# Optimization experiments

Measured on AMD Instinct MI355X. Metric: run time of the kernel, lower is better.

Reference implementation:

```python
import jax, jax.numpy as jnp
import numpy as np

N_NODES = 50000
N_EDGES = 800000
EMB = 128
HID = [128, 128]
OUT = 64
CE = 8  # stand-in for CROSS_ENTROPY_INDEXES: first 8 output columns get sigmoid


def _linear_params(key, d_in, d_out):
    k1, k2 = jax.random.split(key)
    s = 1.0 / np.sqrt(d_in)
    w = jax.random.uniform(k1, (d_in, d_out), minval=-s, maxval=s, dtype=jnp.float32)
    b = jax.random.uniform(k2, (d_out,), minval=-s, maxval=s, dtype=jnp.float32)
    return w, b


def setup_inputs() -> dict:
    key = jax.random.key(0)
    ks = jax.random.split(key, 16)
    z = jax.random.normal(ks[0], (N_NODES, EMB), dtype=jnp.float32)
    edge_index = jax.random.randint(ks[1], (2, N_EDGES), 0, N_NODES, dtype=jnp.int64)
    # SAGEConv params: neighbor weight (with bias) + root weight
    w1_n, b1 = _linear_params(ks[2], EMB, HID[0])
    w1_r, _ = _linear_params(ks[3], EMB, HID[0])
    w2_n, b2 = _linear_params(ks[4], HID[0], HID[1])
    w2_r, _ = _linear_params(ks[5], HID[0], HID[1])
    wf_n, bf = _linear_params(ks[6], HID[1], OUT)
    wf_r, _ = _linear_params(ks[7], HID[1], OUT)
    # initial residual linears: emb -> hid[1], emb -> out
    w_res1, b_res1 = _linear_params(ks[8], EMB, HID[1])
    w_res2, b_res2 = _linear_params(ks[9], EMB, OUT)
    return dict(z=z, edge_index=edge_index,
                w1_n=w1_n, w1_r=w1_r, b1=b1,
                w2_n=w2_n, w2_r=w2_r, b2=b2,
                wf_n=wf_n, wf_r=wf_r, bf=bf,
                w_res1=w_res1, b_res1=b_res1,
                w_res2=w_res2, b_res2=b_res2)


def _sage(x, src, dst, w_n, w_r, b, n_nodes):
    # mean-aggregate neighbor features at target nodes, then affine combine with root
    msg = x[src]                                        # [E, d]
    agg = jax.ops.segment_sum(msg, dst, num_segments=n_nodes)
    deg = jax.ops.segment_sum(jnp.ones_like(dst, dtype=x.dtype), dst, num_segments=n_nodes)
    mean = agg / jnp.maximum(deg, 1.0)[:, None]
    return mean @ w_n + x @ w_r + b


def reference(z, edge_index, w1_n, w1_r, b1, w2_n, w2_r, b2, wf_n, wf_r, bf,
              w_res1, b_res1, w_res2, b_res2):
    n = z.shape[0]
    src, dst = edge_index[0], edge_index[1]
    h = jax.nn.relu(_sage(z, src, dst, w1_n, w1_r, b1, n))
    # mid layer (dropout is identity in eval) + initial residual
    h = jax.nn.relu(_sage(h, src, dst, w2_n, w2_r, b2, n))
    h = h + (z @ w_res1 + b_res1)
    # final conv + final residual
    h = _sage(h, src, dst, wf_n, wf_r, bf, n)
    h = h + (z @ w_res2 + b_res2)
    # sigmoid on cross-entropy columns
    h = h.at[:, :CE].set(jax.nn.sigmoid(h[:, :CE]))
    return h
```

## Files before the change

### kernel.cpp

```cpp
#include <hip/hip_runtime.h>
#include <hip/hip_bf16.h>
#include <math.h>

#define NN 50000
#define NNP 50048
#define NE 800000
#define NB 391
#define EPB 6250

typedef short bf16x8 __attribute__((ext_vector_type(8)));
typedef float f32x4 __attribute__((ext_vector_type(4)));
typedef unsigned short us4 __attribute__((ext_vector_type(4)));
typedef unsigned short us8 __attribute__((ext_vector_type(8)));
typedef unsigned int u32x4 __attribute__((ext_vector_type(4)));

__device__ __forceinline__ float bf2f(unsigned short u) {
  union { unsigned int i; float f; } x; x.i = ((unsigned int)u) << 16; return x.f;
}
__device__ __forceinline__ unsigned short f2bf(float f) {
  union { float f; unsigned int i; } x; x.f = f;
  unsigned int i = x.i;
  unsigned int r = i + 0x7FFF + ((i >> 16) & 1);
  return (unsigned short)(r >> 16);
}
__device__ __forceinline__ unsigned long long pk64(f32x4 v) {
  union { us4 s; unsigned long long u; } x;
  x.s[0] = f2bf(v[0]); x.s[1] = f2bf(v[1]); x.s[2] = f2bf(v[2]); x.s[3] = f2bf(v[3]);
  return x.u;
}

__device__ __forceinline__ int scan_incl_512(int v, int* s) {
  int t = threadIdx.x;
  s[t] = v; __syncthreads();
  for (int off = 1; off < 512; off <<= 1) {
    int x = (t >= off) ? s[t - off] : 0;
    __syncthreads();
    s[t] += x;
    __syncthreads();
  }
  return s[t];
}

__global__ __launch_bounds__(512) void bscat_kernel(const int* __restrict__ srcn,
                                                    const int* __restrict__ dstn,
                                                    const int* __restrict__ bhist,
                                                    int* __restrict__ gcur,
                                                    unsigned long long* __restrict__ ebuf) {
  __shared__ int sbuf[512];
  __shared__ int boff[NB];
  __shared__ int hist[NB];
  __shared__ int base[NB];
  int t = threadIdx.x;
  int v = (t < NB) ? bhist[t] : 0;
  int incl = scan_incl_512(v, sbuf);
  if (t < NB) { boff[t] = incl - v; hist[t] = 0; }
  __syncthreads();
  int e0 = blockIdx.x * EPB;
  for (int i = t; i < EPB; i += 512)
    atomicAdd(&hist[dstn[e0 + i] >> 7], 1);
  __syncthreads();
  for (int i = t; i < NB; i += 512) {
    int c = hist[i];
    base[i] = c ? (boff[i] + atomicAdd(&gcur[i], c)) : 0;
  }
  __syncthreads();
  for (int i = t; i < EPB; i += 512) {
    int s = srcn[e0 + i], d = dstn[e0 + i];
    int b = d >> 7;
    int pos = atomicSub(&hist[b], 1) - 1;
    ebuf[(size_t)base[b] + pos] = ((unsigned long long)(unsigned)d << 32) | (unsigned)s;
  }
}

__global__ __launch_bounds__(512) void bfill_kernel(const unsigned long long* __restrict__ ebuf,
                                                    const int* __restrict__ bhist,
                                                    int* __restrict__ rowoff,
                                                    int* __restrict__ csr) {
  __shared__ int sbuf[512];
  __shared__ int sb[2];
  __shared__ int ndeg[128], noff[128];
  int b = blockIdx.x;
  int t = threadIdx.x;
  int v = (t < NB) ? bhist[t] : 0;
  int incl = scan_incl_512(v, sbuf);
  if (t == b) { sb[0] = incl - v; sb[1] = v; }
  if (t < 128) ndeg[t] = 0;
  __syncthreads();
  int bo = sb[0], cnt = sb[1];
  for (int i = t; i < cnt; i += 512)
    atomicAdd(&ndeg[(int)(ebuf[bo + i] >> 32) & 127], 1);
  __syncthreads();
  if (t < 128) noff[t] = ndeg[t];
  __syncthreads();
  for (int off = 1; off < 128; off <<= 1) {
    int x = 0;
    if (t < 128 && t >= off) x = noff[t - off];
    __syncthreads();
    if (t < 128 && t >= off) noff[t] += x;
    __syncthreads();
  }
  if (t < 128) {
    int ex = noff[t] - ndeg[t];
    noff[t] = ex;
    int node = b * 128 + t;
    if (node < NN) rowoff[node] = bo + ex;
  }
  if (b == NB - 1 && t == 0) rowoff[NN] = NE;
  __syncthreads();
  for (int i = t; i < cnt; i += 512) {
    unsigned long long e = ebuf[bo + i];
    int dl = (int)(e >> 32) & 127;
    int pos = atomicSub(&ndeg[dl], 1) - 1;
    csr[bo + noff[dl] + pos] = (int)(unsigned)e;
  }
}

__global__ __launch_bounds__(256) void setup_kernel(
    const float* __restrict__ z, unsigned short* __restrict__ Z16,
    const float* __restrict__ w1n, const float* __restrict__ w1r,
    const float* __restrict__ w2n, const float* __restrict__ w2r,
    const float* __restrict__ wfn, const float* __restrict__ wfr,
    const float* __restrict__ wr1, const float* __restrict__ wr2,
    unsigned short* __restrict__ Bp1, unsigned short* __restrict__ Bp2,
    unsigned short* __restrict__ Bp3,
    const int* __restrict__ dstn, int* __restrict__ bhist) {
  __shared__ int h[NB];
  int b = blockIdx.x;
  if (b < 6250) {
    int i = b * 256 + threadIdx.x;
    if (i >= NN * 128 / 4) return;
    int i4 = i * 4;
    int row = i4 >> 7, c = i4 & 127;
    f32x4 v = *(const f32x4*)(z + i4);
    us4 o = { f2bf(v[0]), f2bf(v[1]), f2bf(v[2]), f2bf(v[3]) };
    *(us4*)(Z16 + (size_t)row * 128 + c) = o;
  } else if (b < 6314) {
    int g = (b - 6250) * 256 + threadIdx.x;
    unsigned short* D; int NT, fi;
    int which;
    if      (g < 10240) { fi = g;         D = Bp1; NT = 20; which = 1; }
    else if (g < 14336) { fi = g - 10240; D = Bp2; NT = 8;  which = 2; }
    else if (g < 16384) { fi = g - 14336; D = Bp3; NT = 4;  which = 3; }
    else return;
    int lane = fi & 63, t = fi >> 6;
    int nt = t % NT, k0i = t / NT;
    int m = lane & 15, q = lane >> 4;
    int kb = k0i * 32 + q * 8;
    int n = nt * 16 + m;
    int hi = (kb >= 128);
    int k0_ = kb - (hi ? 128 : 0);
    const float* W = nullptr; int Nseg = 128; int nn = n;
    if (which == 1) {
      if (n < 128)      { W = hi ? w1r : w1n; nn = n; Nseg = 128; }
      else if (n < 256) { W = hi ? wr1 : nullptr; nn = n - 128; Nseg = 128; }
      else              { W = hi ? wr2 : nullptr; nn = n - 256; Nseg = 64; }
    } else if (which == 2) { W = hi ? w2r : w2n; Nseg = 128; }
    else                   { W = hi ? wfr : wfn; Nseg = 64; }
    unsigned short o[8];
#pragma unroll
    for (int j = 0; j < 8; j++)
      o[j] = W ? f2bf(W[(size_t)(k0_ + j) * Nseg + nn]) : (unsigned short)0;
    *(us8*)(D + (size_t)fi * 8) = *(const us8*)o;
  } else {
    for (int i = threadIdx.x; i < NB; i += 256) h[i] = 0;
    __syncthreads();
    int e0 = (b - 6314) * EPB;
    for (int i = threadIdx.x; i < EPB; i += 256)
      atomicAdd(&h[dstn[e0 + i] >> 7], 1);
    __syncthreads();
    for (int i = threadIdx.x; i < NB; i += 256)
      if (h[i]) atomicAdd(&bhist[i], h[i]);
  }
}

__device__ __forceinline__ void gather_mean(const unsigned short* __restrict__ feat,
                                            int row0,
                                            const int* __restrict__ rowoff,
                                            const int* __restrict__ csr,
                                            unsigned short* meanS) {
  int tid = threadIdx.x;
  int w = tid >> 6, lane = tid & 63;
  int g = lane >> 4;
  int c = (lane & 15) << 3;
#pragma unroll 2
  for (int i = 0; i < 16; ++i) {
    int node = row0 + w * 16 + i;
    int beg = 0, end = 0;
    if (node < NN) { beg = rowoff[node]; end = rowoff[node + 1]; }
    float a[8];
#pragma unroll
    for (int k = 0; k < 8; ++k) a[k] = 0.f;
    int e1 = end - 1;
    for (int j = beg + g; j < end; j += 16) {
      int j1 = (j + 4 < e1) ? j + 4 : e1;
      int j2 = (j + 8 < e1) ? j + 8 : e1;
      int j3 = (j + 12 < e1) ? j + 12 : e1;
      int s0 = csr[j], s1 = csr[j1], s2 = csr[j2], s3 = csr[j3];
      float w1 = (j + 4 < end) ? 1.f : 0.f;
      float w2 = (j + 8 < end) ? 1.f : 0.f;
      float w3 = (j + 12 < end) ? 1.f : 0.f;
      u32x4 v0 = *(const u32x4*)(feat + (size_t)s0 * 128 + c);
      u32x4 v1 = *(const u32x4*)(feat + (size_t)s1 * 128 + c);
      u32x4 v2 = *(const u32x4*)(feat + (size_t)s2 * 128 + c);
      u32x4 v3 = *(const u32x4*)(feat + (size_t)s3 * 128 + c);
#pragma unroll
      for (int k = 0; k < 4; ++k) {
        float l0 = bf2f((unsigned short)(v0[k] & 0xffff));
        float h0 = bf2f((unsigned short)(v0[k] >> 16));
        l0 = fmaf(w1, bf2f((unsigned short)(v1[k] & 0xffff)), l0);
        h0 = fmaf(w1, bf2f((unsigned short)(v1[k] >> 16)), h0);
        l0 = fmaf(w2, bf2f((unsigned short)(v2[k] & 0xffff)), l0);
        h0 = fmaf(w2, bf2f((unsigned short)(v2[k] >> 16)), h0);
        l0 = fmaf(w3, bf2f((unsigned short)(v3[k] & 0xffff)), l0);
        h0 = fmaf(w3, bf2f((unsigned short)(v3[k] >> 16)), h0);
        a[2 * k] += l0;
        a[2 * k + 1] += h0;
      }
    }
#pragma unroll
    for (int k = 0; k < 8; ++k) {
      a[k] += __shfl_xor(a[k], 16, 64);
      a[k] += __shfl_xor(a[k], 32, 64);
    }
    if (g == 0) {
      float inv = 1.f / fmaxf((float)(end - beg), 1.f);
      unsigned int o[4];
#pragma unroll
      for (int k = 0; k < 4; ++k)
        o[k] = ((unsigned int)f2bf(a[2 * k + 1] * inv) << 16) | f2bf(a[2 * k] * inv);
      int rl = w * 16 + i;
      int byte = rl * 256 + (c << 1);
      byte ^= ((i & 7) << 4);
      *(u32x4*)((char*)meanS + byte) = *(const u32x4*)o;
    }
  }
}

__device__ __forceinline__ bf16x8 mean_frag(const unsigned short* meanS,
                                            int w, int m, int q, int k0i) {
  int rl = w * 16 + m;
  int byte = rl * 256 + q * 16 + k0i * 64;
  byte ^= ((m & 7) << 4);
  return *(const bf16x8*)((const char*)meanS + byte);
}

__device__ __forceinline__ void stage_B(unsigned short* Bs, const unsigned short* __restrict__ Bp,
                                        int k0i, int T, int NTfull, int tid) {
  for (int i = tid; i < T * 64; i += 512) {
    int t = i >> 6, r = i & 63;
    *(us8*)(Bs + (size_t)t * 512 + (size_t)r * 8) =
        *(const us8*)(Bp + ((size_t)(k0i * NTfull + t)) * 512 + (size_t)r * 8);
  }
}

__global__ __launch_bounds__(512, 4) void fused1_kernel(
    const unsigned short* __restrict__ Z16,
    const unsigned short* __restrict__ Bp,
    const float* __restrict__ b1, const float* __restrict__ br1, const float* __restrict__ br2,
    const int* __restrict__ rowoff, const int* __restrict__ csr,
    unsigned short* __restrict__ h1, unsigned short* __restrict__ res1,
    unsigned short* __restrict__ res2)
{
  __shared__ unsigned short meanS[128 * 128];
  __shared__ unsigned short Bs[20 * 512];
  int tid = threadIdx.x;
  int w = tid >> 6, lane = tid & 63;
  int m = lane & 15, q = lane >> 4;
  int row0 = blockIdx.x * 128;
  int row = row0 + w * 16 + m;
  bf16x8 afx[4];
  const unsigned short* xr = Z16 + (size_t)row * 128 + q * 8;
#pragma unroll
  for (int k = 0; k < 4; ++k) afx[k] = *(const bf16x8*)(xr + k * 32);
  stage_B(Bs, Bp, 0, 8, 20, tid);
  gather_mean(Z16, row0, rowoff, csr, meanS);
  __syncthreads();
  f32x4 acc[20];
#pragma unroll
  for (int t = 0; t < 20; ++t) acc[t] = (f32x4){0.f, 0.f, 0.f, 0.f};
#pragma unroll
  for (int k0i = 0; k0i < 8; ++k0i) {
    const unsigned short* bk = Bs + lane * 8;
    if (k0i < 4) {
      bf16x8 af = mean_frag(meanS, w, m, q, k0i);
#pragma unroll
      for (int t = 0; t < 8; ++t)
        acc[t] = __builtin_amdgcn_mfma_f32_16x16x32_bf16(*(const bf16x8*)(bk + t * 512), af, acc[t], 0, 0, 0);
    } else {
      bf16x8 af = afx[k0i - 4];
#pragma unroll
      for (int t = 0; t < 20; ++t)
        acc[t] = __builtin_amdgcn_mfma_f32_16x16x32_bf16(*(const bf16x8*)(bk + t * 512), af, acc[t], 0, 0, 0);
    }
    __syncthreads();
    if (k0i < 7) {
      stage_B(Bs, Bp, k0i + 1, (k0i + 1 < 4) ? 8 : 20, 20, tid);
      __syncthreads();
    }
  }
  int src0 = m + ((q & 1) ? 32 : 0);
#pragma unroll
  for (int p = 0; p < 10; ++p) {
    const float* bias; unsigned short* dst; int dstride, colb, relu;
    if (p < 4)      { bias = b1  + 32 * p;       dst = h1;   dstride = 128; colb = 32 * p;       relu = 1; }
    else if (p < 8) { bias = br1 + 32 * (p - 4); dst = res1; dstride = 128; colb = 32 * (p - 4); relu = 0; }
    else            { bias = br2 + 32 * (p - 8); dst = res2; dstride = 64;  colb = 32 * (p - 8); relu = 0; }
    f32x4 v0 = acc[2 * p], v1 = acc[2 * p + 1];
    f32x4 bb0 = *(const f32x4*)(bias + 4 * q);
    f32x4 bb1 = *(const f32x4*)(bias + 16 + 4 * q);
#pragma unroll
    for (int r = 0; r < 4; ++r) { v0[r] += bb0[r]; v1[r] += bb1[r]; }
    if (relu) {
#pragma unroll
      for (int r = 0; r < 4; ++r) { v0[r] = fmaxf(v0[r], 0.f); v1[r] = fmaxf(v1[r], 0.f); }
    }
    unsigned long long d0 = pk64(v0), d1 = pk64(v1);
    unsigned long long a0 = __shfl(d0, src0, 64);
    unsigned long long b0 = __shfl(d0, src0 + 16, 64);
    unsigned long long a1 = __shfl(d1, src0, 64);
    unsigned long long b1v = __shfl(d1, src0 + 16, 64);
    unsigned long long lo = (q >> 1) ? a1 : a0;
    unsigned long long hi = (q >> 1) ? b1v : b0;
    if (row < NN) {
      unsigned long long ov[2] = { lo, hi };
      *(us8*)(dst + (size_t)row * dstride + colb + 8 * q) = *(const us8*)ov;
    }
  }
}

__global__ __launch_bounds__(512, 4) void fused2_kernel(
    const unsigned short* __restrict__ H1,
    const unsigned short* __restrict__ Bp,
    const float* __restrict__ b2,
    const int* __restrict__ rowoff, const int* __restrict__ csr,
    const unsigned short* __restrict__ res1,
    unsigned short* __restrict__ h2)
{
  __shared__ unsigned short meanS[128 * 128];
  __shared__ unsigned short Bs[8 * 512];
  int tid = threadIdx.x;
  int w = tid >> 6, lane = tid & 63;
  int m = lane & 15, q = lane >> 4;
  int row0 = blockIdx.x * 128;
  int row = row0 + w * 16 + m;
  bf16x8 afx[4];
  const unsigned short* xr = H1 + (size_t)row * 128 + q * 8;
#pragma unroll
  for (int k = 0; k < 4; ++k) afx[k] = *(const bf16x8*)(xr + k * 32);
  stage_B(Bs, Bp, 0, 8, 8, tid);
  gather_mean(H1, row0, rowoff, csr, meanS);
  __syncthreads();
  f32x4 acc[8];
#pragma unroll
  for (int t = 0; t < 8; ++t) acc[t] = (f32x4){0.f, 0.f, 0.f, 0.f};
#pragma unroll
  for (int k0i = 0; k0i < 8; ++k0i) {
    const unsigned short* bk = Bs + lane * 8;
    bf16x8 af = (k0i < 4) ? mean_frag(meanS, w, m, q, k0i) : afx[k0i - 4];
#pragma unroll
    for (int t = 0; t < 8; ++t)
      acc[t] = __builtin_amdgcn_mfma_f32_16x16x32_bf16(*(const bf16x8*)(bk + t * 512), af, acc[t], 0, 0, 0);
    __syncthreads();
    if (k0i < 7) {
      stage_B(Bs, Bp, k0i + 1, 8, 8, tid);
      __syncthreads();
    }
  }
  int src0 = m + ((q & 1) ? 32 : 0);
#pragma unroll
  for (int p = 0; p < 4; ++p) {
    f32x4 v0 = acc[2 * p], v1 = acc[2 * p + 1];
    f32x4 bb0 = *(const f32x4*)(b2 + 32 * p + 4 * q);
    f32x4 bb1 = *(const f32x4*)(b2 + 32 * p + 16 + 4 * q);
#pragma unroll
    for (int r = 0; r < 4; ++r) {
      v0[r] = fmaxf(v0[r] + bb0[r], 0.f);
      v1[r] = fmaxf(v1[r] + bb1[r], 0.f);
    }
    unsigned long long d0 = pk64(v0), d1 = pk64(v1);
    unsigned long long a0 = __shfl(d0, src0, 64);
    unsigned long long b0 = __shfl(d0, src0 + 16, 64);
    unsigned long long a1 = __shfl(d1, src0, 64);
    unsigned long long b1v = __shfl(d1, src0 + 16, 64);
    unsigned long long lo = (q >> 1) ? a1 : a0;
    unsigned long long hi = (q >> 1) ? b1v : b0;
    if (row < NN) {
      size_t off = 32 * p + 8 * q;
      us8 rv = *(const us8*)(res1 + (size_t)row * 128 + off);
      unsigned long long ov[2] = { lo, hi };
      unsigned short* e = (unsigned short*)ov;
#pragma unroll
      for (int r = 0; r < 8; ++r) e[r] = f2bf(bf2f(e[r]) + bf2f(rv[r]));
      *(us8*)(h2 + (size_t)row * 128 + off) = *(const us8*)ov;
    }
  }
}

__global__ __launch_bounds__(512, 4) void fused3_kernel(
    const unsigned short* __restrict__ H2,
    const unsigned short* __restrict__ Bp,
    const float* __restrict__ bias,
    const int* __restrict__ rowoff, const int* __restrict__ csr,
    const unsigned short* __restrict__ res2,
    float* __restrict__ out_f)
{
  __shared__ unsigned short meanS[128 * 128];
  __shared__ unsigned short Bs[4 * 512];
  int tid = threadIdx.x;
  int w = tid >> 6, lane = tid & 63;
  int m = lane & 15, q = lane >> 4;
  int row0 = blockIdx.x * 128;
  int row = row0 + w * 16 + m;
  bf16x8 afx[4];
  const unsigned short* xr = H2 + (size_t)row * 128 + q * 8;
#pragma unroll
  for (int k = 0; k < 4; ++k) afx[k] = *(const bf16x8*)(xr + k * 32);
  stage_B(Bs, Bp, 0, 4, 4, tid);
  gather_mean(H2, row0, rowoff, csr, meanS);
  __syncthreads();
  f32x4 acc[4];
#pragma unroll
  for (int t = 0; t < 4; ++t) acc[t] = (f32x4){0.f, 0.f, 0.f, 0.f};
#pragma unroll
  for (int k0i = 0; k0i < 8; ++k0i) {
    const unsigned short* bk = Bs + lane * 8;
    bf16x8 af = (k0i < 4) ? mean_frag(meanS, w, m, q, k0i) : afx[k0i - 4];
#pragma unroll
    for (int t = 0; t < 4; ++t)
      acc[t] = __builtin_amdgcn_mfma_f32_16x16x32_bf16(*(const bf16x8*)(bk + t * 512), af, acc[t], 0, 0, 0);
    __syncthreads();
    if (k0i < 7) {
      stage_B(Bs, Bp, k0i + 1, 4, 4, tid);
      __syncthreads();
    }
  }
  if (row >= NN) return;
  int cb = q * 4;
#pragma unroll
  for (int s = 0; s < 4; ++s) {
    int col = s * 16 + cb;
    f32x4 v = acc[s];
    f32x4 bb = *(const f32x4*)(bias + col);
    us4 rv = *(const us4*)(res2 + (size_t)row * 64 + col);
#pragma unroll
    for (int r = 0; r < 4; ++r) v[r] += bb[r] + bf2f(rv[r]);
    if (col < 8) {
#pragma unroll
      for (int r = 0; r < 4; ++r) v[r] = 1.f / (1.f + __expf(-v[r]));
    }
    *(f32x4*)(out_f + (size_t)row * 64 + col) = v;
  }
}

extern "C" void kernel_launch(void* const* d_in, const int* in_sizes, int n_in,
                              void* d_out, int out_size, void* d_ws, size_t ws_size,
                              hipStream_t stream) {
  const float* z   = (const float*)d_in[0];
  const int*   edge = (const int*)d_in[1];
  const int*   srcn = edge;
  const int*   dstn = edge + NE;
  const float* w1n = (const float*)d_in[2];
  const float* w1r = (const float*)d_in[3];
  const float* b1  = (const float*)d_in[4];
  const float* w2n = (const float*)d_in[5];
  const float* w2r = (const float*)d_in[6];
  const float* b2  = (const float*)d_in[7];
  const float* wfn = (const float*)d_in[8];
  const float* wfr = (const float*)d_in[9];
  const float* bfb = (const float*)d_in[10];
  const float* wr1 = (const float*)d_in[11];
  const float* br1 = (const float*)d_in[12];
  const float* wr2 = (const float*)d_in[13];
  const float* br2 = (const float*)d_in[14];
  float* out = (float*)d_out;

  char* p = (char*)d_ws;
  auto alloc = [&](size_t bytes) { char* r = p; p += (bytes + 255) & ~255ull; return r; };
  int* rowoff = (int*)alloc((size_t)(NN + 1) * 4);
  int* bhist  = (int*)alloc((size_t)2 * NB * 4);
  int* gcur   = bhist + NB;
  int* csr    = (int*)alloc((size_t)NE * 4);
  unsigned short* Z16 = (unsigned short*)alloc((size_t)NNP * 128 * 2);
  unsigned short* H1  = (unsigned short*)alloc((size_t)NNP * 128 * 2);
  unsigned short* H2  = (unsigned short*)alloc((size_t)NNP * 128 * 2);
  unsigned short* res1 = (unsigned short*)alloc((size_t)NN * 128 * 2);
  unsigned short* res2 = (unsigned short*)alloc((size_t)NN * 64 * 2);
  unsigned short* Bp1 = (unsigned short*)alloc(10240 * 8 * 2);
  unsigned short* Bp2 = (unsigned short*)alloc(4096 * 8 * 2);
  unsigned short* Bp3 = (unsigned short*)alloc(2048 * 8 * 2);
  unsigned long long* ebuf = (unsigned long long*)res1;

  hipMemsetAsync(bhist, 0, (size_t)2 * NB * 4, stream);
  setup_kernel<<<6442, 256, 0, stream>>>(z, Z16, w1n, w1r, w2n, w2r, wfn, wfr, wr1, wr2,
                                         Bp1, Bp2, Bp3, dstn, bhist);
  bscat_kernel<<<128, 512, 0, stream>>>(srcn, dstn, bhist, gcur, ebuf);
  bfill_kernel<<<NB, 512, 0, stream>>>(ebuf, bhist, rowoff, csr);

  const int gy = NNP / 128;

  fused1_kernel<<<gy, 512, 0, stream>>>(Z16, Bp1, b1, br1, br2, rowoff, csr, H1, res1, res2);
  fused2_kernel<<<gy, 512, 0, stream>>>(H1, Bp2, b2, rowoff, csr, res1, H2);
  fused3_kernel<<<gy, 512, 0, stream>>>(H2, Bp3, bfb, rowoff, csr, res2, out);
}
```

Baseline: 296.1 us.

## Split fused SAGE layers into separate aggregation and GEMM kernels with concatenated layout

Each fused gather+GEMM kernel is split in two. A wave-per-node aggregation kernel writes the neighbour mean into the left half of a [N,256] bf16 buffer whose right half holds the node features. A GEMM kernel then reads contiguous 256-wide rows and takes B fragments straight from global memory, with no LDS staging or block barriers. The layer-1 residual GEMMs run as extra blocks alongside the first aggregation. This trades the tail imbalance and large-LDS occupancy limits of the fused kernels for extra launches and a write and re-read of the mean through global memory.

```diff
diff --git a/kernel.cpp b/kernel.cpp
--- a/kernel.cpp
+++ b/kernel.cpp
@@ -27,6 +27,9 @@
   union { us4 s; unsigned long long u; } x;
   x.s[0] = f2bf(v[0]); x.s[1] = f2bf(v[1]); x.s[2] = f2bf(v[2]); x.s[3] = f2bf(v[3]);
   return x.u;
+}
+__device__ __forceinline__ bf16x8 bfrag(const unsigned short* __restrict__ Bp, int idx, int lane) {
+  return *(const bf16x8*)(Bp + (size_t)idx * 512 + lane * 8);
 }
 
 __device__ __forceinline__ int scan_incl_512(int v, int* s) {
@@ -116,7 +119,7 @@
 }
 
 __global__ __launch_bounds__(256) void setup_kernel(
-    const float* __restrict__ z, unsigned short* __restrict__ Z16,
+    const float* __restrict__ z, unsigned short* __restrict__ A1,
     const float* __restrict__ w1n, const float* __restrict__ w1r,
     const float* __restrict__ w2n, const float* __restrict__ w2r,
     const float* __restrict__ wfn, const float* __restrict__ wfr,
@@ -133,7 +136,7 @@
     int row = i4 >> 7, c = i4 & 127;
     f32x4 v = *(const f32x4*)(z + i4);
     us4 o = { f2bf(v[0]), f2bf(v[1]), f2bf(v[2]), f2bf(v[3]) };
-    *(us4*)(Z16 + (size_t)row * 128 + c) = o;
+    *(us4*)(A1 + (size_t)row * 256 + 128 + c) = o;
   } else if (b < 6314) {
     int g = (b - 6250) * 256 + threadIdx.x;
     unsigned short* D; int NT, fi;
@@ -173,147 +176,111 @@
   }
 }
 
-__device__ __forceinline__ void gather_mean(const unsigned short* __restrict__ feat,
-                                            int row0,
-                                            const int* __restrict__ rowoff,
-                                            const int* __restrict__ csr,
-                                            unsigned short* meanS) {
-  int tid = threadIdx.x;
-  int w = tid >> 6, lane = tid & 63;
+__device__ __forceinline__ void agg_wave(const unsigned short* __restrict__ feat,
+                                         unsigned short* __restrict__ outm,
+                                         const int* __restrict__ rowoff,
+                                         const int* __restrict__ csr, int node) {
+  int lane = threadIdx.x & 63;
   int g = lane >> 4;
   int c = (lane & 15) << 3;
-#pragma unroll 2
-  for (int i = 0; i < 16; ++i) {
-    int node = row0 + w * 16 + i;
-    int beg = 0, end = 0;
-    if (node < NN) { beg = rowoff[node]; end = rowoff[node + 1]; }
-    float a[8];
-#pragma unroll
-    for (int k = 0; k < 8; ++k) a[k] = 0.f;
-    int e1 = end - 1;
-    for (int j = beg + g; j < end; j += 16) {
-      int j1 = (j + 4 < e1) ? j + 4 : e1;
-      int j2 = (j + 8 < e1) ? j + 8 : e1;
-      int j3 = (j + 12 < e1) ? j + 12 : e1;
-      int s0 = csr[j], s1 = csr[j1], s2 = csr[j2], s3 = csr[j3];
-      float w1 = (j + 4 < end) ? 1.f : 0.f;
-      float w2 = (j + 8 < end) ? 1.f : 0.f;
-      float w3 = (j + 12 < end) ? 1.f : 0.f;
-      u32x4 v0 = *(const u32x4*)(feat + (size_t)s0 * 128 + c);
-      u32x4 v1 = *(const u32x4*)(feat + (size_t)s1 * 128 + c);
-      u32x4 v2 = *(const u32x4*)(feat + (size_t)s2 * 128 + c);
-      u32x4 v3 = *(const u32x4*)(feat + (size_t)s3 * 128 + c);
-#pragma unroll
-      for (int k = 0; k < 4; ++k) {
-        float l0 = bf2f((unsigned short)(v0[k] & 0xffff));
-        float h0 = bf2f((unsigned short)(v0[k] >> 16));
-        l0 = fmaf(w1, bf2f((unsigned short)(v1[k] & 0xffff)), l0);
-        h0 = fmaf(w1, bf2f((unsigned short)(v1[k] >> 16)), h0);
-        l0 = fmaf(w2, bf2f((unsigned short)(v2[k] & 0xffff)), l0);
-        h0 = fmaf(w2, bf2f((unsigned short)(v2[k] >> 16)), h0);
-        l0 = fmaf(w3, bf2f((unsigned short)(v3[k] & 0xffff)), l0);
-        h0 = fmaf(w3, bf2f((unsigned short)(v3[k] >> 16)), h0);
-        a[2 * k] += l0;
-        a[2 * k + 1] += h0;
-      }
-    }
-#pragma unroll
-    for (int k = 0; k < 8; ++k) {
-      a[k] += __shfl_xor(a[k], 16, 64);
-      a[k] += __shfl_xor(a[k], 32, 64);
-    }
-    if (g == 0) {
-      float inv = 1.f / fmaxf((float)(end - beg), 1.f);
-      unsigned int o[4];
-#pragma unroll
-      for (int k = 0; k < 4; ++k)
-        o[k] = ((unsigned int)f2bf(a[2 * k + 1] * inv) << 16) | f2bf(a[2 * k] * inv);
-      int rl = w * 16 + i;
-      int byte = rl * 256 + (c << 1);
-      byte ^= ((i & 7) << 4);
-      *(u32x4*)((char*)meanS + byte) = *(const u32x4*)o;
-    }
-  }
-}
-
-__device__ __forceinline__ bf16x8 mean_frag(const unsigned short* meanS,
-                                            int w, int m, int q, int k0i) {
-  int rl = w * 16 + m;
-  int byte = rl * 256 + q * 16 + k0i * 64;
-  byte ^= ((m & 7) << 4);
-  return *(const bf16x8*)((const char*)meanS + byte);
-}
-
-__device__ __forceinline__ void stage_B(unsigned short* Bs, const unsigned short* __restrict__ Bp,
-                                        int k0i, int T, int NTfull, int tid) {
-  for (int i = tid; i < T * 64; i += 512) {
-    int t = i >> 6, r = i & 63;
-    *(us8*)(Bs + (size_t)t * 512 + (size_t)r * 8) =
-        *(const us8*)(Bp + ((size_t)(k0i * NTfull + t)) * 512 + (size_t)r * 8);
-  }
-}
-
-__global__ __launch_bounds__(512, 4) void fused1_kernel(
-    const unsigned short* __restrict__ Z16,
-    const unsigned short* __restrict__ Bp,
-    const float* __restrict__ b1, const float* __restrict__ br1, const float* __restrict__ br2,
+  if (node >= NN) return;
+  int beg = rowoff[node], end = rowoff[node + 1];
+  float a[8];
+#pragma unroll
+  for (int i = 0; i < 8; i++) a[i] = 0.f;
+  int e1 = end - 1;
+  for (int j = beg + g; j < end; j += 16) {
+    int j1 = (j + 4 < e1) ? j + 4 : e1;
+    int j2 = (j + 8 < e1) ? j + 8 : e1;
+    int j3 = (j + 12 < e1) ? j + 12 : e1;
+    int s0 = csr[j], s1 = csr[j1], s2 = csr[j2], s3 = csr[j3];
+    float w1 = (j + 4 < end) ? 1.f : 0.f;
+    float w2 = (j + 8 < end) ? 1.f : 0.f;
+    float w3 = (j + 12 < end) ? 1.f : 0.f;
+    u32x4 v0 = *(const u32x4*)(feat + (size_t)s0 * 256 + c);
+    u32x4 v1 = *(const u32x4*)(feat + (size_t)s1 * 256 + c);
+    u32x4 v2 = *(const u32x4*)(feat + (size_t)s2 * 256 + c);
+    u32x4 v3 = *(const u32x4*)(feat + (size_t)s3 * 256 + c);
+#pragma unroll
+    for (int i = 0; i < 4; i++) {
+      float l0 = bf2f((unsigned short)(v0[i] & 0xffff));
+      float h0 = bf2f((unsigned short)(v0[i] >> 16));
+      l0 = fmaf(w1, bf2f((unsigned short)(v1[i] & 0xffff)), l0);
+      h0 = fmaf(w1, bf2f((unsigned short)(v1[i] >> 16)), h0);
+      l0 = fmaf(w2, bf2f((unsigned short)(v2[i] & 0xffff)), l0);
+      h0 = fmaf(w2, bf2f((unsigned short)(v2[i] >> 16)), h0);
+      l0 = fmaf(w3, bf2f((unsigned short)(v3[i] & 0xffff)), l0);
+      h0 = fmaf(w3, bf2f((unsigned short)(v3[i] >> 16)), h0);
+      a[2*i] += l0;
+      a[2*i+1] += h0;
+    }
+  }
+#pragma unroll
+  for (int i = 0; i < 8; i++) {
+    a[i] += __shfl_xor(a[i], 16, 64);
+    a[i] += __shfl_xor(a[i], 32, 64);
+  }
+  if (g == 0) {
+    float inv = 1.f / fmaxf((float)(end - beg), 1.f);
+    unsigned int o[4];
+#pragma unroll
+    for (int i = 0; i < 4; i++)
+      o[i] = ((unsigned int)f2bf(a[2*i+1] * inv) << 16) | f2bf(a[2*i] * inv);
+    *(u32x4*)(outm + (size_t)node * 256 + c) = *(const u32x4*)o;
+  }
+}
+
+__global__ __launch_bounds__(512, 8) void agg_kernel(unsigned short* __restrict__ A,
+                                                     const int* __restrict__ rowoff,
+                                                     const int* __restrict__ csr) {
+  int node = blockIdx.x * 8 + (threadIdx.x >> 6);
+  agg_wave(A + 128, A, rowoff, csr, node);
+}
+
+__global__ __launch_bounds__(512, 4) void aggres1_kernel(
+    unsigned short* __restrict__ A1,
+    const unsigned short* __restrict__ Bp1,
+    const float* __restrict__ br1, const float* __restrict__ br2,
     const int* __restrict__ rowoff, const int* __restrict__ csr,
-    unsigned short* __restrict__ h1, unsigned short* __restrict__ res1,
-    unsigned short* __restrict__ res2)
-{
-  __shared__ unsigned short meanS[128 * 128];
-  __shared__ unsigned short Bs[20 * 512];
+    unsigned short* __restrict__ res1, unsigned short* __restrict__ res2) {
+  int bx = blockIdx.x;
+  if (bx < 6250) {
+    int node = bx * 8 + (threadIdx.x >> 6);
+    agg_wave(A1 + 128, A1, rowoff, csr, node);
+    return;
+  }
+  int b = bx - 6250;
+  int chunk = (b >= NB);
+  int bb = b - chunk * NB;
   int tid = threadIdx.x;
   int w = tid >> 6, lane = tid & 63;
   int m = lane & 15, q = lane >> 4;
-  int row0 = blockIdx.x * 128;
-  int row = row0 + w * 16 + m;
-  bf16x8 afx[4];
-  const unsigned short* xr = Z16 + (size_t)row * 128 + q * 8;
-#pragma unroll
-  for (int k = 0; k < 4; ++k) afx[k] = *(const bf16x8*)(xr + k * 32);
-  stage_B(Bs, Bp, 0, 8, 20, tid);
-  gather_mean(Z16, row0, rowoff, csr, meanS);
-  __syncthreads();
-  f32x4 acc[20];
-#pragma unroll
-  for (int t = 0; t < 20; ++t) acc[t] = (f32x4){0.f, 0.f, 0.f, 0.f};
-#pragma unroll
-  for (int k0i = 0; k0i < 8; ++k0i) {
-    const unsigned short* bk = Bs + lane * 8;
-    if (k0i < 4) {
-      bf16x8 af = mean_frag(meanS, w, m, q, k0i);
-#pragma unroll
-      for (int t = 0; t < 8; ++t)
-        acc[t] = __builtin_amdgcn_mfma_f32_16x16x32_bf16(*(const bf16x8*)(bk + t * 512), af, acc[t], 0, 0, 0);
-    } else {
-      bf16x8 af = afx[k0i - 4];
-#pragma unroll
-      for (int t = 0; t < 20; ++t)
-        acc[t] = __builtin_amdgcn_mfma_f32_16x16x32_bf16(*(const bf16x8*)(bk + t * 512), af, acc[t], 0, 0, 0);
-    }
-    __syncthreads();
-    if (k0i < 7) {
-      stage_B(Bs, Bp, k0i + 1, (k0i + 1 < 4) ? 8 : 20, 20, tid);
-      __syncthreads();
-    }
-  }
+  int row = bb * 128 + w * 16 + m;
+  const unsigned short* ar = A1 + (size_t)row * 256 + 128 + q * 8;
+  bf16x8 af[4];
+#pragma unroll
+  for (int k = 0; k < 4; ++k) af[k] = *(const bf16x8*)(ar + k * 32);
+  f32x4 acc[6];
+#pragma unroll
+  for (int t = 0; t < 6; ++t) acc[t] = (f32x4){0.f, 0.f, 0.f, 0.f};
+#pragma unroll
+  for (int k0i = 0; k0i < 4; ++k0i)
+#pragma unroll
+    for (int t = 0; t < 6; ++t)
+      acc[t] = __builtin_amdgcn_mfma_f32_16x16x32_bf16(
+          bfrag(Bp1, (k0i + 4) * 20 + 8 + chunk * 6 + t, lane), af[k0i], acc[t], 0, 0, 0);
   int src0 = m + ((q & 1) ? 32 : 0);
 #pragma unroll
-  for (int p = 0; p < 10; ++p) {
-    const float* bias; unsigned short* dst; int dstride, colb, relu;
-    if (p < 4)      { bias = b1  + 32 * p;       dst = h1;   dstride = 128; colb = 32 * p;       relu = 1; }
-    else if (p < 8) { bias = br1 + 32 * (p - 4); dst = res1; dstride = 128; colb = 32 * (p - 4); relu = 0; }
-    else            { bias = br2 + 32 * (p - 8); dst = res2; dstride = 64;  colb = 32 * (p - 8); relu = 0; }
-    f32x4 v0 = acc[2 * p], v1 = acc[2 * p + 1];
+  for (int pl = 0; pl < 3; ++pl) {
+    int P = chunk * 3 + pl;
+    const float* bias; unsigned short* dst; int dstride, colb;
+    if (P < 4) { bias = br1 + 32 * P;       dst = res1; dstride = 128; colb = 32 * P; }
+    else       { bias = br2 + 32 * (P - 4); dst = res2; dstride = 64;  colb = 32 * (P - 4); }
+    f32x4 v0 = acc[2 * pl], v1 = acc[2 * pl + 1];
     f32x4 bb0 = *(const f32x4*)(bias + 4 * q);
     f32x4 bb1 = *(const f32x4*)(bias + 16 + 4 * q);
 #pragma unroll
     for (int r = 0; r < 4; ++r) { v0[r] += bb0[r]; v1[r] += bb1[r]; }
-    if (relu) {
-#pragma unroll
-      for (int r = 0; r < 4; ++r) { v0[r] = fmaxf(v0[r], 0.f); v1[r] = fmaxf(v1[r], 0.f); }
-    }
     unsigned long long d0 = pk64(v0), d1 = pk64(v1);
     unsigned long long a0 = __shfl(d0, src0, 64);
     unsigned long long b0 = __shfl(d0, src0 + 16, 64);
@@ -328,44 +295,76 @@
   }
 }
 
-__global__ __launch_bounds__(512, 4) void fused2_kernel(
-    const unsigned short* __restrict__ H1,
-    const unsigned short* __restrict__ Bp,
-    const float* __restrict__ b2,
-    const int* __restrict__ rowoff, const int* __restrict__ csr,
-    const unsigned short* __restrict__ res1,
-    unsigned short* __restrict__ h2)
-{
-  __shared__ unsigned short meanS[128 * 128];
-  __shared__ unsigned short Bs[8 * 512];
+__global__ __launch_bounds__(512) void gemm1h_kernel(
+    const unsigned short* __restrict__ A1,
+    const unsigned short* __restrict__ Bp1,
+    const float* __restrict__ b1,
+    unsigned short* __restrict__ A2) {
   int tid = threadIdx.x;
   int w = tid >> 6, lane = tid & 63;
   int m = lane & 15, q = lane >> 4;
-  int row0 = blockIdx.x * 128;
-  int row = row0 + w * 16 + m;
-  bf16x8 afx[4];
-  const unsigned short* xr = H1 + (size_t)row * 128 + q * 8;
-#pragma unroll
-  for (int k = 0; k < 4; ++k) afx[k] = *(const bf16x8*)(xr + k * 32);
-  stage_B(Bs, Bp, 0, 8, 8, tid);
-  gather_mean(H1, row0, rowoff, csr, meanS);
-  __syncthreads();
+  int row = blockIdx.x * 128 + w * 16 + m;
+  const unsigned short* ar = A1 + (size_t)row * 256 + q * 8;
+  bf16x8 af[8];
+#pragma unroll
+  for (int k = 0; k < 8; ++k) af[k] = *(const bf16x8*)(ar + k * 32);
   f32x4 acc[8];
 #pragma unroll
   for (int t = 0; t < 8; ++t) acc[t] = (f32x4){0.f, 0.f, 0.f, 0.f};
 #pragma unroll
-  for (int k0i = 0; k0i < 8; ++k0i) {
-    const unsigned short* bk = Bs + lane * 8;
-    bf16x8 af = (k0i < 4) ? mean_frag(meanS, w, m, q, k0i) : afx[k0i - 4];
+  for (int k0i = 0; k0i < 8; ++k0i)
 #pragma unroll
     for (int t = 0; t < 8; ++t)
-      acc[t] = __builtin_amdgcn_mfma_f32_16x16x32_bf16(*(const bf16x8*)(bk + t * 512), af, acc[t], 0, 0, 0);
-    __syncthreads();
-    if (k0i < 7) {
-      stage_B(Bs, Bp, k0i + 1, 8, 8, tid);
-      __syncthreads();
-    }
-  }
+      acc[t] = __builtin_amdgcn_mfma_f32_16x16x32_bf16(
+          bfrag(Bp1, k0i * 20 + t, lane), af[k0i], acc[t], 0, 0, 0);
+  int src0 = m + ((q & 1) ? 32 : 0);
+#pragma unroll
+  for (int p = 0; p < 4; ++p) {
+    f32x4 v0 = acc[2 * p], v1 = acc[2 * p + 1];
+    f32x4 bb0 = *(const f32x4*)(b1 + 32 * p + 4 * q);
+    f32x4 bb1 = *(const f32x4*)(b1 + 32 * p + 16 + 4 * q);
+#pragma unroll
+    for (int r = 0; r < 4; ++r) {
+      v0[r] = fmaxf(v0[r] + bb0[r], 0.f);
+      v1[r] = fmaxf(v1[r] + bb1[r], 0.f);
+    }
+    unsigned long long d0 = pk64(v0), d1 = pk64(v1);
+    unsigned long long a0 = __shfl(d0, src0, 64);
+    unsigned long long b0 = __shfl(d0, src0 + 16, 64);
+    unsigned long long a1 = __shfl(d1, src0, 64);
+    unsigned long long b1v = __shfl(d1, src0 + 16, 64);
+    unsigned long long lo = (q >> 1) ? a1 : a0;
+    unsigned long long hi = (q >> 1) ? b1v : b0;
+    if (row < NN) {
+      unsigned long long ov[2] = { lo, hi };
+      *(us8*)(A2 + (size_t)row * 256 + 128 + 32 * p + 8 * q) = *(const us8*)ov;
+    }
+  }
+}
+
+__global__ __launch_bounds__(512) void gemm2_kernel(
+    const unsigned short* __restrict__ A2,
+    const unsigned short* __restrict__ Bp2,
+    const float* __restrict__ b2,
+    const unsigned short* __restrict__ res1,
+    unsigned short* __restrict__ A3) {
+  int tid = threadIdx.x;
+  int w = tid >> 6, lane = tid & 63;
+  int m = lane & 15, q = lane >> 4;
+  int row = blockIdx.x * 128 + w * 16 + m;
+  const unsigned short* ar = A2 + (size_t)row * 256 + q * 8;
+  bf16x8 af[8];
+#pragma unroll
+  for (int k = 0; k < 8; ++k) af[k] = *(const bf16x8*)(ar + k * 32);
+  f32x4 acc[8];
+#pragma unroll
+  for (int t = 0; t < 8; ++t) acc[t] = (f32x4){0.f, 0.f, 0.f, 0.f};
+#pragma unroll
+  for (int k0i = 0; k0i < 8; ++k0i)
+#pragma unroll
+    for (int t = 0; t < 8; ++t)
+      acc[t] = __builtin_amdgcn_mfma_f32_16x16x32_bf16(
+          bfrag(Bp2, k0i * 8 + t, lane), af[k0i], acc[t], 0, 0, 0);
   int src0 = m + ((q & 1) ? 32 : 0);
 #pragma unroll
   for (int p = 0; p < 4; ++p) {
@@ -391,49 +390,34 @@
       unsigned short* e = (unsigned short*)ov;
 #pragma unroll
       for (int r = 0; r < 8; ++r) e[r] = f2bf(bf2f(e[r]) + bf2f(rv[r]));
-      *(us8*)(h2 + (size_t)row * 128 + off) = *(const us8*)ov;
-    }
-  }
-}
-
-__global__ __launch_bounds__(512, 4) void fused3_kernel(
-    const unsigned short* __restrict__ H2,
-    const unsigned short* __restrict__ Bp,
+      *(us8*)(A3 + (size_t)row * 256 + 128 + off) = *(const us8*)ov;
+    }
+  }
+}
+
+__global__ __launch_bounds__(512) void gemm3_kernel(
+    const unsigned short* __restrict__ A3,
+    const unsigned short* __restrict__ Bp3,
     const float* __restrict__ bias,
-    const int* __restrict__ rowoff, const int* __restrict__ csr,
     const unsigned short* __restrict__ res2,
-    float* __restrict__ out_f)
-{
-  __shared__ unsigned short meanS[128 * 128];
-  __shared__ unsigned short Bs[4 * 512];
+    float* __restrict__ out_f) {
   int tid = threadIdx.x;
   int w = tid >> 6, lane = tid & 63;
   int m = lane & 15, q = lane >> 4;
-  int row0 = blockIdx.x * 128;
-  int row = row0 + w * 16 + m;
-  bf16x8 afx[4];
-  const unsigned short* xr = H2 + (size_t)row * 128 + q * 8;
-#pragma unroll
-  for (int k = 0; k < 4; ++k) afx[k] = *(const bf16x8*)(xr + k * 32);
-  stage_B(Bs, Bp, 0, 4, 4, tid);
-  gather_mean(H2, row0, rowoff, csr, meanS);
-  __syncthreads();
+  int row = blockIdx.x * 128 + w * 16 + m;
+  const unsigned short* ar = A3 + (size_t)row * 256 + q * 8;
+  bf16x8 af[8];
+#pragma unroll
+  for (int k = 0; k < 8; ++k) af[k] = *(const bf16x8*)(ar + k * 32);
   f32x4 acc[4];
 #pragma unroll
   for (int t = 0; t < 4; ++t) acc[t] = (f32x4){0.f, 0.f, 0.f, 0.f};
 #pragma unroll
-  for (int k0i = 0; k0i < 8; ++k0i) {
-    const unsigned short* bk = Bs + lane * 8;
-    bf16x8 af = (k0i < 4) ? mean_frag(meanS, w, m, q, k0i) : afx[k0i - 4];
+  for (int k0i = 0; k0i < 8; ++k0i)
 #pragma unroll
     for (int t = 0; t < 4; ++t)
-      acc[t] = __builtin_amdgcn_mfma_f32_16x16x32_bf16(*(const bf16x8*)(bk + t * 512), af, acc[t], 0, 0, 0);
-    __syncthreads();
-    if (k0i < 7) {
-      stage_B(Bs, Bp, k0i + 1, 4, 4, tid);
-      __syncthreads();
-    }
-  }
+      acc[t] = __builtin_amdgcn_mfma_f32_16x16x32_bf16(
+          bfrag(Bp3, k0i * 4 + t, lane), af[k0i], acc[t], 0, 0, 0);
   if (row >= NN) return;
   int cb = q * 4;
 #pragma unroll
@@ -480,25 +464,28 @@
   int* bhist  = (int*)alloc((size_t)2 * NB * 4);
   int* gcur   = bhist + NB;
   int* csr    = (int*)alloc((size_t)NE * 4);
-  unsigned short* Z16 = (unsigned short*)alloc((size_t)NNP * 128 * 2);
-  unsigned short* H1  = (unsigned short*)alloc((size_t)NNP * 128 * 2);
-  unsigned short* H2  = (unsigned short*)alloc((size_t)NNP * 128 * 2);
+  unsigned short* A1 = (unsigned short*)alloc((size_t)NNP * 256 * 2);
+  unsigned short* A2 = (unsigned short*)alloc((size_t)NNP * 256 * 2);
   unsigned short* res1 = (unsigned short*)alloc((size_t)NN * 128 * 2);
   unsigned short* res2 = (unsigned short*)alloc((size_t)NN * 64 * 2);
   unsigned short* Bp1 = (unsigned short*)alloc(10240 * 8 * 2);
   unsigned short* Bp2 = (unsigned short*)alloc(4096 * 8 * 2);
   unsigned short* Bp3 = (unsigned short*)alloc(2048 * 8 * 2);
+  unsigned short* A3 = A1;
   unsigned long long* ebuf = (unsigned long long*)res1;
 
   hipMemsetAsync(bhist, 0, (size_t)2 * NB * 4, stream);
-  setup_kernel<<<6442, 256, 0, stream>>>(z, Z16, w1n, w1r, w2n, w2r, wfn, wfr, wr1, wr2,
+  setup_kernel<<<6442, 256, 0, stream>>>(z, A1, w1n, w1r, w2n, w2r, wfn, wfr, wr1, wr2,
                                          Bp1, Bp2, Bp3, dstn, bhist);
   bscat_kernel<<<128, 512, 0, stream>>>(srcn, dstn, bhist, gcur, ebuf);
   bfill_kernel<<<NB, 512, 0, stream>>>(ebuf, bhist, rowoff, csr);
 
-  const int gy = NNP / 128;
-
-  fused1_kernel<<<gy, 512, 0, stream>>>(Z16, Bp1, b1, br1, br2, rowoff, csr, H1, res1, res2);
-  fused2_kernel<<<gy, 512, 0, stream>>>(H1, Bp2, b2, rowoff, csr, res1, H2);
-  fused3_kernel<<<gy, 512, 0, stream>>>(H2, Bp3, bfb, rowoff, csr, res2, out);
-}
+  aggres1_kernel<<<6250 + 2 * NB, 512, 0, stream>>>(A1, Bp1, br1, br2, rowoff, csr, res1, res2);
+  gemm1h_kernel<<<NB, 512, 0, stream>>>(A1, Bp1, b1, A2);
+
+  agg_kernel<<<6250, 512, 0, stream>>>(A2, rowoff, csr);
+  gemm2_kernel<<<NB, 512, 0, stream>>>(A2, Bp2, b2, res1, A3);
+
+  agg_kernel<<<6250, 512, 0, stream>>>(A3, rowoff, csr);
+  gemm3_kernel<<<NB, 512, 0, stream>>>(A3, Bp3, bfb, res2, out);
+}
```

Result: faster. 279.8 us (-5.5%).
